# Kernel optimization log

Hardware: AMD Instinct MI355X
Metric: run time of the kernel (lower is better)

## Reference

```python
import jax, jax.numpy as jnp
import numpy as np

M = 28            # mask head resolution (mask_logit[i] is MxM)
NUM_CLASSES = 80  # max value of cls_idx (mask_image channel count)


def setup_inputs() -> dict:
    key = jax.random.key(0)
    k1, k2, k3, k4, k5, k6, k7 = jax.random.split(key, 7)
    N, H, W = 100, 800, 800
    cx = jax.random.uniform(k1, (N,), minval=0.0, maxval=float(W - 1))
    cy = jax.random.uniform(k2, (N,), minval=0.0, maxval=float(H - 1))
    bw = jax.random.uniform(k3, (N,), minval=20.0, maxval=300.0)
    bh = jax.random.uniform(k4, (N,), minval=20.0, maxval=300.0)
    mask_rois = jnp.stack([cx - bw / 2, cy - bh / 2, cx + bw / 2, cy + bh / 2], axis=1).astype(jnp.float32)
    cls_prob = jax.random.uniform(k5, (N,), dtype=jnp.float32)
    mask_prob = jax.random.normal(k6, (N, M, M), dtype=jnp.float32)
    cls_idx = jax.random.randint(k7, (N,), 1, NUM_CLASSES + 1, dtype=jnp.int32)
    return {"mask_rois": mask_rois, "cls_prob": cls_prob, "mask_prob": mask_prob,
            "cls_idx": cls_idx, "im_h": H, "im_w": W}


def _paste(logit, box, H, W):
    """Bilinear-paste an MxM logit into the full HxW image (== cv2.resize to (w,h)
    then placing at the box, evaluated directly on image pixel coords)."""
    x0, y0, x1, y1 = box[0], box[1], box[2], box[3]  # int32
    w = jnp.maximum(x1 - x0 + 1, 1).astype(jnp.float32)
    h = jnp.maximum(y1 - y0 + 1, 1).astype(jnp.float32)
    xs = jnp.arange(W, dtype=jnp.float32)
    ys = jnp.arange(H, dtype=jnp.float32)
    # cv2 bilinear mapping: src = (dst + 0.5) * (M / size) - 0.5, clamped at borders
    sx = jnp.clip((xs - x0.astype(jnp.float32) + 0.5) * (M / w) - 0.5, 0.0, M - 1.0)
    sy = jnp.clip((ys - y0.astype(jnp.float32) + 0.5) * (M / h) - 0.5, 0.0, M - 1.0)
    ix0 = jnp.floor(sx).astype(jnp.int32); ix1 = jnp.minimum(ix0 + 1, M - 1); fx = sx - ix0
    iy0 = jnp.floor(sy).astype(jnp.int32); iy1 = jnp.minimum(iy0 + 1, M - 1); fy = sy - iy0
    v00 = logit[iy0[:, None], ix0[None, :]]
    v01 = logit[iy0[:, None], ix1[None, :]]
    v10 = logit[iy1[:, None], ix0[None, :]]
    v11 = logit[iy1[:, None], ix1[None, :]]
    val = ((1 - fy)[:, None] * ((1 - fx)[None, :] * v00 + fx[None, :] * v01)
           + fy[:, None] * ((1 - fx)[None, :] * v10 + fx[None, :] * v11))
    xi = jnp.arange(W, dtype=jnp.int32)
    yi = jnp.arange(H, dtype=jnp.int32)
    inside_x = (xi >= jnp.maximum(x0, 0)) & (xi < jnp.minimum(x1 + 1, W))
    inside_y = (yi >= jnp.maximum(y0, 0)) & (yi < jnp.minimum(y1 + 1, H))
    inside = inside_y[:, None] & inside_x[None, :]
    return jnp.where(inside, val, 0.0), inside


def _forward(mask_rois, cls_prob, mask_prob, cls_idx, H, W, thr):
    N = mask_prob.shape[0]
    order = jnp.argsort(-cls_prob)                       # sort by score, descending
    boxes = mask_rois[order].astype(jnp.int32)
    logits = mask_prob[order]
    cls = cls_idx[order].astype(jnp.int32) - 1           # 0-based class ids
    pasted, inside = jax.vmap(lambda l, b: _paste(l, b, H, W))(logits, boxes)  # [N,H,W]

    def step(mask_image, xs):
        logit, ins, c = xs
        mask = (logit > 0) & ins                          # thresholded, in-image crop mask
        prev = mask_image[c]
        msum = jnp.sum(mask).astype(jnp.float32)
        ovl = jnp.sum(mask & prev).astype(jnp.float32)    # overlap with accumulated class mask
        keep = (msum > 0) & (ovl <= thr * msum)           # skip if ratio > threshold
        mask_image = mask_image.at[c].set(prev | (mask & keep))
        return mask_image, keep

    mask_image0 = jnp.zeros((NUM_CLASSES, H, W), dtype=bool)
    _, keep = jax.lax.scan(step, mask_image0, (pasted, inside, cls))

    # compact kept masks to the front (frame_id order); dropped boxes go to slot N (discarded)
    pos = jnp.where(keep, jnp.cumsum(keep.astype(jnp.int32)) - 1, N)
    energy = jnp.where(inside & keep[:, None, None], pasted, 0.0)
    full = jnp.zeros((N + 1, H, W), pasted.dtype).at[pos].set(energy)
    mask_energy = full[:N][None]                          # [1, N, H, W], kept masks first
    keep_inds = jnp.full((N + 1,), -1, jnp.int32).at[pos].set(
        jnp.where(keep, order.astype(jnp.int32), -1))[:N]
    return keep_inds, mask_energy


def reference(mask_rois, cls_prob, mask_prob, cls_idx, im_h, im_w):
    return _forward(mask_rois, cls_prob, mask_prob, cls_idx, int(im_h), int(im_w), 0.3)
```

## Files before the change

### kernel.cpp

```cpp
#include <hip/hip_runtime.h>

#define NINST 100
#define MLOG 28
#define IMG 800
#define LOGSZ (MLOG * MLOG)

#define OFF_ORDER 0
#define OFF_CLS   100
#define OFF_BOX   200
#define OFF_MSUM  600
#define OFF_SLOT  800
#define OFF_NK    900
#define OFF_NPAIR 901
#define OFF_MASK  1024
#define ROWW      12
#define MSTRIDE   (ROWW * 304)
#define OFF_PAIRS (OFF_MASK + NINST * MSTRIDE)
#define PAIR_CAP  512
#define ZTOT      (IMG * IMG * NINST / 4)
#define ZGRID     4096

__global__ __launch_bounds__(256) void k_raster(const float* __restrict__ mask_prob,
                                                const float* __restrict__ cls_prob,
                                                const float* __restrict__ rois,
                                                const int* __restrict__ cls_idx,
                                                int* __restrict__ ws) {
    int b = blockIdx.x, tid = threadIdx.x;
    __shared__ float s_p[NINST];
    __shared__ int s_order[NINST];
    __shared__ float lg[LOGSZ];
    __shared__ int red[256];
    if (tid < NINST) s_p[tid] = cls_prob[tid];
    __syncthreads();
    if (tid < NINST) {
        float p = s_p[tid];
        int r = 0;
        for (int j = 0; j < NINST; j++) {
            float q = s_p[j];
            r += (q > p) || (q == p && j < tid);
        }
        s_order[r] = tid;
    }
    __syncthreads();
    int n = b;
    int orig = s_order[n];
    int x0 = (int)rois[4 * orig], y0 = (int)rois[4 * orig + 1];
    int x1 = (int)rois[4 * orig + 2], y1 = (int)rois[4 * orig + 3];
    if (b == 0) {
        if (tid == 0) ws[OFF_NPAIR] = 0;
        if (tid < NINST) {
            int o = s_order[tid];
            ws[OFF_ORDER + tid] = o;
            ws[OFF_CLS + tid] = cls_idx[o] - 1;
#pragma unroll
            for (int k = 0; k < 4; k++)
                ws[OFF_BOX + 4 * tid + k] = (int)rois[4 * o + k];
        }
    }
    for (int i = tid; i < LOGSZ; i += 256) lg[i] = mask_prob[orig * LOGSZ + i];
    __syncthreads();
    int xs = max(x0, 0), xe = min(x1 + 1, IMG);
    int ys = max(y0, 0), ye = min(y1 + 1, IMG);
    int wx0 = xs >> 5, nw = ((xe + 31) >> 5) - wx0, nrows = ye - ys;
    float wf = fmaxf((float)(x1 - x0 + 1), 1.f), hf = fmaxf((float)(y1 - y0 + 1), 1.f);
    float rx = 28.f / wf, ry = 28.f / hf;
    unsigned* mb = (unsigned*)(ws + OFF_MASK) + n * MSTRIDE;
    int total = nrows * nw, cnt = 0;
    for (int t = tid; t < total; t += 256) {
        int row = t / nw, wc = t - row * nw;
        int y = ys + row;
        float sy = ((float)y - (float)y0 + 0.5f) * ry - 0.5f;
        sy = fminf(fmaxf(sy, 0.f), 27.f);
        int iy0 = (int)sy, iy1 = min(iy0 + 1, 27);
        float fy = sy - (float)iy0;
        const float* r0 = lg + iy0 * MLOG;
        const float* r1 = lg + iy1 * MLOG;
        unsigned bits = 0u;
        int xbase = (wx0 + wc) << 5;
        int j0 = max(xs - xbase, 0), j1 = min(xe - xbase, 32);
        for (int j = j0; j < j1; j++) {
            int xx = xbase + j;
            float sx = ((float)xx - (float)x0 + 0.5f) * rx - 0.5f;
            sx = fminf(fmaxf(sx, 0.f), 27.f);
            int ix0 = (int)sx, ix1 = min(ix0 + 1, 27);
            float fx = sx - (float)ix0;
            float val = (1.f - fy) * ((1.f - fx) * r0[ix0] + fx * r0[ix1]) +
                        fy * ((1.f - fx) * r1[ix0] + fx * r1[ix1]);
            bits |= (val > 0.f) ? (1u << j) : 0u;
        }
        mb[row * ROWW + wc] = bits;
        cnt += __popc(bits);
    }
    red[tid] = cnt;
    __syncthreads();
    for (int s = 128; s; s >>= 1) {
        if (tid < s) red[tid] += red[tid + s];
        __syncthreads();
    }
    if (tid == 0) ws[OFF_MSUM + n] = red[0];
}

__global__ __launch_bounds__(64) void k_pairs(int* __restrict__ ws) {
    int i = blockIdx.x, j = blockIdx.y, tid = threadIdx.x;
    if (i >= j) return;
    if (ws[OFF_CLS + i] != ws[OFF_CLS + j]) return;
    if (ws[OFF_MSUM + i] == 0 || ws[OFF_MSUM + j] == 0) return;
    const int* bi = ws + OFF_BOX + 4 * i;
    const int* bj = ws + OFF_BOX + 4 * j;
    int ixs = max(bi[0], 0), ixe = min(bi[2] + 1, IMG);
    int iys = max(bi[1], 0), iye = min(bi[3] + 1, IMG);
    int jxs = max(bj[0], 0), jxe = min(bj[2] + 1, IMG);
    int jys = max(bj[1], 0), jye = min(bj[3] + 1, IMG);
    if (!(ixs < jxe && jxs < ixe && iys < jye && jys < iye)) return;
    int iwx0 = ixs >> 5, jwx0 = jxs >> 5;
    int wlo = max(iwx0, jwx0);
    int whi = min((ixe + 31) >> 5, (jxe + 31) >> 5);
    int rlo = max(iys, jys), rhi = min(iye, jye);
    int nw = whi - wlo, nrows = rhi - rlo;
    const unsigned* mi = (const unsigned*)(ws + OFF_MASK) + i * MSTRIDE;
    const unsigned* mj = (const unsigned*)(ws + OFF_MASK) + j * MSTRIDE;
    int total = nrows * nw, cnt = 0;
    for (int t = tid; t < total; t += 64) {
        int row = t / nw, wc = t - row * nw;
        int y = rlo + row, w = wlo + wc;
        unsigned a = mi[(y - iys) * ROWW + (w - iwx0)];
        unsigned b = mj[(y - jys) * ROWW + (w - jwx0)];
        cnt += __popc(a & b);
    }
    for (int off = 32; off; off >>= 1) cnt += __shfl_down(cnt, off);
    if (tid == 0) {
        int k = atomicAdd(ws + OFF_NPAIR, 1);
        if (k < PAIR_CAP) {
            ws[OFF_PAIRS + 3 * k] = i;
            ws[OFF_PAIRS + 3 * k + 1] = j;
            ws[OFF_PAIRS + 3 * k + 2] = cnt;
        }
    }
}

__global__ __launch_bounds__(256) void k_scan_zero(int* __restrict__ ws, float* __restrict__ out) {
    int b = blockIdx.x, tid = threadIdx.x;
    if (b > 0) {
        float4* z = (float4*)(out + NINST);
        for (size_t pi = (size_t)(b - 1) * 256 + tid; pi < (size_t)ZTOT; pi += (size_t)ZGRID * 256)
            z[pi] = make_float4(0.f, 0.f, 0.f, 0.f);
        return;
    }
    __shared__ int s_box[4 * NINST];
    __shared__ int s_msum[NINST];
    __shared__ int s_keep[NINST];
    __shared__ int s_cand[32];
    __shared__ int s_ncand, s_sum, s_max, s_need;
    __shared__ int s_pi[PAIR_CAP], s_pj[PAIR_CAP], s_po[PAIR_CAP];
    __shared__ int red[256];
    for (int i = tid; i < NINST; i += 256) s_msum[i] = ws[OFF_MSUM + i];
    for (int i = tid; i < 4 * NINST; i += 256) s_box[i] = ws[OFF_BOX + i];
    int npair = min(ws[OFF_NPAIR], PAIR_CAP);
    for (int i = tid; i < npair; i += 256) {
        s_pi[i] = ws[OFF_PAIRS + 3 * i];
        s_pj[i] = ws[OFF_PAIRS + 3 * i + 1];
        s_po[i] = ws[OFF_PAIRS + 3 * i + 2];
    }
    const unsigned* maskbase = (const unsigned*)(ws + OFF_MASK);
    __syncthreads();

    for (int n = 0; n < NINST; n++) {
        if (tid == 0) { s_ncand = 0; s_sum = 0; s_max = 0; }
        __syncthreads();
        for (int q = tid; q < npair; q += 256) {
            if (s_pj[q] == n && s_keep[s_pi[q]]) {
                int k = atomicAdd(&s_ncand, 1);
                if (k < 32) s_cand[k] = s_pi[q];
                atomicAdd(&s_sum, s_po[q]);
                atomicMax(&s_max, s_po[q]);
            }
        }
        __syncthreads();
        if (tid == 0) {
            int msum = s_msum[n];
            float t = 0.3f * (float)msum;
            int keep, need = 0;
            if (s_ncand == 0 || (float)s_sum <= t) keep = (msum > 0);
            else if ((float)s_max > t) keep = 0;
            else { keep = 0; need = 1; }
            s_keep[n] = keep;
            s_need = need;
        }
        __syncthreads();
        if (s_need) {
            int nc = min(s_ncand, 32);
            int nxs = max(s_box[4 * n], 0), nxe = min(s_box[4 * n + 2] + 1, IMG);
            int nys = max(s_box[4 * n + 1], 0), nye = min(s_box[4 * n + 3] + 1, IMG);
            int wx0 = nxs >> 5, nw = ((nxe + 31) >> 5) - wx0, nrows = nye - nys;
            const unsigned* mn = maskbase + n * MSTRIDE;
            int total = nrows * nw, ovl = 0;
            for (int t2 = tid; t2 < total; t2 += 256) {
                int row = t2 / nw, wc = t2 - row * nw;
                unsigned bits = mn[row * ROWW + wc];
                if (!bits) continue;
                int y = nys + row, wa = wx0 + wc;
                unsigned img = 0;
                for (int k = 0; k < nc; k++) {
                    int m = s_cand[k];
                    int mys = max(s_box[4 * m + 1], 0), mye = min(s_box[4 * m + 3] + 1, IMG);
                    int mxs = max(s_box[4 * m], 0), mxe = min(s_box[4 * m + 2] + 1, IMG);
                    int mwx0 = mxs >> 5, mnw = ((mxe + 31) >> 5) - mwx0;
                    int rr = y - mys, cc = wa - mwx0;
                    if (rr >= 0 && rr < (mye - mys) && cc >= 0 && cc < mnw)
                        img |= maskbase[m * MSTRIDE + rr * ROWW + cc];
                }
                ovl += __popc(bits & img);
            }
            red[tid] = ovl;
            __syncthreads();
            for (int s = 128; s; s >>= 1) {
                if (tid < s) red[tid] += red[tid + s];
                __syncthreads();
            }
            if (tid == 0) {
                int msum = s_msum[n];
                s_keep[n] = (msum > 0) && ((float)red[0] <= 0.3f * (float)msum);
            }
        }
    }
    __syncthreads();
    if (tid == 0) {
        int nk = 0;
        for (int n = 0; n < NINST; n++) {
            if (s_keep[n]) {
                ws[OFF_SLOT + nk] = n;
                out[nk] = (float)ws[OFF_ORDER + n];
                nk++;
            }
        }
        ws[OFF_NK] = nk;
        for (int s = nk; s < NINST; s++) out[s] = -1.f;
    }
}

__global__ __launch_bounds__(256) void k_box(const float* __restrict__ mask_prob,
                                             const int* __restrict__ ws,
                                             float* __restrict__ out) {
    int slot = blockIdx.y, tid = threadIdx.x;
    if (slot >= ws[OFF_NK]) return;
    int n = ws[OFF_SLOT + slot];
    const int* box = ws + OFF_BOX + 4 * n;
    int x0 = box[0], y0 = box[1], x1 = box[2], y1 = box[3];
    int xs = max(x0, 0), xe = min(x1 + 1, IMG);
    int ys = max(y0, 0), ye = min(y1 + 1, IMG);
    int xa = xs & ~3;
    int w4 = (xe - xa + 3) >> 2;
    int rows = ye - ys;
    int total = rows * w4;
    __shared__ float lg[LOGSZ];
    int orig = ws[OFF_ORDER + n];
    for (int i = tid; i < LOGSZ; i += 256) lg[i] = mask_prob[orig * LOGSZ + i];
    __syncthreads();
    float wf = fmaxf((float)(x1 - x0 + 1), 1.f), hf = fmaxf((float)(y1 - y0 + 1), 1.f);
    float rx = 28.f / wf, ry = 28.f / hf;
    float* base = out + NINST + (size_t)slot * (IMG * IMG);
    for (int t = blockIdx.x * 256 + tid; t < total; t += gridDim.x * 256) {
        int row = t / w4, c4 = t - row * w4;
        int y = ys + row, xb = xa + (c4 << 2);
        float sy = ((float)y - (float)y0 + 0.5f) * ry - 0.5f;
        sy = fminf(fmaxf(sy, 0.f), 27.f);
        int iy0 = (int)sy, iy1 = min(iy0 + 1, 27);
        float fy = sy - (float)iy0;
        const float* r0 = lg + iy0 * MLOG;
        const float* r1 = lg + iy1 * MLOG;
        float v[4];
#pragma unroll
        for (int j = 0; j < 4; j++) {
            int xx = xb + j;
            float val = 0.f;
            if (xx >= xs && xx < xe) {
                float sx = ((float)xx - (float)x0 + 0.5f) * rx - 0.5f;
                sx = fminf(fmaxf(sx, 0.f), 27.f);
                int ix0 = (int)sx, ix1 = min(ix0 + 1, 27);
                float fx = sx - (float)ix0;
                val = (1.f - fy) * ((1.f - fx) * r0[ix0] + fx * r0[ix1]) +
                      fy * ((1.f - fx) * r1[ix0] + fx * r1[ix1]);
            }
            v[j] = val;
        }
        *(float4*)(base + (size_t)y * IMG + xb) = make_float4(v[0], v[1], v[2], v[3]);
    }
}

extern "C" void kernel_launch(void* const* d_in, const int* in_sizes, int n_in,
                              void* d_out, int out_size, void* d_ws, size_t ws_size,
                              hipStream_t stream) {
    const float* rois      = (const float*)d_in[0];
    const float* cls_prob  = (const float*)d_in[1];
    const float* mask_prob = (const float*)d_in[2];
    const int*   cls_idx   = (const int*)d_in[3];
    int* ws = (int*)d_ws;
    float* out = (float*)d_out;

    k_raster<<<dim3(NINST), dim3(256), 0, stream>>>(mask_prob, cls_prob, rois, cls_idx, ws);
    k_pairs<<<dim3(NINST, NINST), dim3(64), 0, stream>>>(ws);
    k_scan_zero<<<dim3(1 + ZGRID), dim3(256), 0, stream>>>(ws, out);
    k_box<<<dim3(91, NINST), dim3(256), 0, stream>>>(mask_prob, ws, out);
}
```

Before: 331.8 us.

## Fuse four kernels into one persistent kernel with grid-wide atomic barriers

Result: slower. 625.1 us (+88.4%).

```diff
diff --git a/kernel.cpp b/kernel.cpp
--- a/kernel.cpp
+++ b/kernel.cpp
@@ -12,278 +12,310 @@
 #define OFF_SLOT  800
 #define OFF_NK    900
 #define OFF_NPAIR 901
+#define OFF_BAR   904
 #define OFF_MASK  1024
 #define ROWW      12
 #define MSTRIDE   (ROWW * 304)
 #define OFF_PAIRS (OFF_MASK + NINST * MSTRIDE)
 #define PAIR_CAP  512
 #define ZTOT      (IMG * IMG * NINST / 4)
-#define ZGRID     4096
-
-__global__ __launch_bounds__(256) void k_raster(const float* __restrict__ mask_prob,
+#define GRID      1024
+#define BOXTILES  91
+#define BOXVTOT   (NINST * BOXTILES)
+#define BOXCHUNK  ((BOXVTOT + GRID - 1) / GRID)
+
+__device__ __forceinline__ void gbar(int* cnt) {
+    __syncthreads();
+    if (threadIdx.x == 0) {
+        __threadfence();
+        atomicAdd(cnt, 1);
+        while (__hip_atomic_load(cnt, __ATOMIC_RELAXED, __HIP_MEMORY_SCOPE_AGENT) < GRID)
+            __builtin_amdgcn_s_sleep(8);
+        __threadfence();
+    }
+    __syncthreads();
+}
+
+__global__ __launch_bounds__(256, 4) void k_all(const float* __restrict__ mask_prob,
                                                 const float* __restrict__ cls_prob,
                                                 const float* __restrict__ rois,
                                                 const int* __restrict__ cls_idx,
-                                                int* __restrict__ ws) {
+                                                int* __restrict__ ws,
+                                                float* __restrict__ out) {
     int b = blockIdx.x, tid = threadIdx.x;
     __shared__ float s_p[NINST];
     __shared__ int s_order[NINST];
     __shared__ float lg[LOGSZ];
     __shared__ int red[256];
-    if (tid < NINST) s_p[tid] = cls_prob[tid];
-    __syncthreads();
-    if (tid < NINST) {
-        float p = s_p[tid];
-        int r = 0;
-        for (int j = 0; j < NINST; j++) {
-            float q = s_p[j];
-            r += (q > p) || (q == p && j < tid);
-        }
-        s_order[r] = tid;
-    }
-    __syncthreads();
-    int n = b;
-    int orig = s_order[n];
-    int x0 = (int)rois[4 * orig], y0 = (int)rois[4 * orig + 1];
-    int x1 = (int)rois[4 * orig + 2], y1 = (int)rois[4 * orig + 3];
-    if (b == 0) {
-        if (tid == 0) ws[OFF_NPAIR] = 0;
-        if (tid < NINST) {
-            int o = s_order[tid];
-            ws[OFF_ORDER + tid] = o;
-            ws[OFF_CLS + tid] = cls_idx[o] - 1;
-#pragma unroll
-            for (int k = 0; k < 4; k++)
-                ws[OFF_BOX + 4 * tid + k] = (int)rois[4 * o + k];
-        }
-    }
-    for (int i = tid; i < LOGSZ; i += 256) lg[i] = mask_prob[orig * LOGSZ + i];
-    __syncthreads();
-    int xs = max(x0, 0), xe = min(x1 + 1, IMG);
-    int ys = max(y0, 0), ye = min(y1 + 1, IMG);
-    int wx0 = xs >> 5, nw = ((xe + 31) >> 5) - wx0, nrows = ye - ys;
-    float wf = fmaxf((float)(x1 - x0 + 1), 1.f), hf = fmaxf((float)(y1 - y0 + 1), 1.f);
-    float rx = 28.f / wf, ry = 28.f / hf;
-    unsigned* mb = (unsigned*)(ws + OFF_MASK) + n * MSTRIDE;
-    int total = nrows * nw, cnt = 0;
-    for (int t = tid; t < total; t += 256) {
-        int row = t / nw, wc = t - row * nw;
-        int y = ys + row;
-        float sy = ((float)y - (float)y0 + 0.5f) * ry - 0.5f;
-        sy = fminf(fmaxf(sy, 0.f), 27.f);
-        int iy0 = (int)sy, iy1 = min(iy0 + 1, 27);
-        float fy = sy - (float)iy0;
-        const float* r0 = lg + iy0 * MLOG;
-        const float* r1 = lg + iy1 * MLOG;
-        unsigned bits = 0u;
-        int xbase = (wx0 + wc) << 5;
-        int j0 = max(xs - xbase, 0), j1 = min(xe - xbase, 32);
-        for (int j = j0; j < j1; j++) {
-            int xx = xbase + j;
-            float sx = ((float)xx - (float)x0 + 0.5f) * rx - 0.5f;
-            sx = fminf(fmaxf(sx, 0.f), 27.f);
-            int ix0 = (int)sx, ix1 = min(ix0 + 1, 27);
-            float fx = sx - (float)ix0;
-            float val = (1.f - fy) * ((1.f - fx) * r0[ix0] + fx * r0[ix1]) +
-                        fy * ((1.f - fx) * r1[ix0] + fx * r1[ix1]);
-            bits |= (val > 0.f) ? (1u << j) : 0u;
-        }
-        mb[row * ROWW + wc] = bits;
-        cnt += __popc(bits);
-    }
-    red[tid] = cnt;
-    __syncthreads();
-    for (int s = 128; s; s >>= 1) {
-        if (tid < s) red[tid] += red[tid + s];
-        __syncthreads();
-    }
-    if (tid == 0) ws[OFF_MSUM + n] = red[0];
-}
-
-__global__ __launch_bounds__(64) void k_pairs(int* __restrict__ ws) {
-    int i = blockIdx.x, j = blockIdx.y, tid = threadIdx.x;
-    if (i >= j) return;
-    if (ws[OFF_CLS + i] != ws[OFF_CLS + j]) return;
-    if (ws[OFF_MSUM + i] == 0 || ws[OFF_MSUM + j] == 0) return;
-    const int* bi = ws + OFF_BOX + 4 * i;
-    const int* bj = ws + OFF_BOX + 4 * j;
-    int ixs = max(bi[0], 0), ixe = min(bi[2] + 1, IMG);
-    int iys = max(bi[1], 0), iye = min(bi[3] + 1, IMG);
-    int jxs = max(bj[0], 0), jxe = min(bj[2] + 1, IMG);
-    int jys = max(bj[1], 0), jye = min(bj[3] + 1, IMG);
-    if (!(ixs < jxe && jxs < ixe && iys < jye && jys < iye)) return;
-    int iwx0 = ixs >> 5, jwx0 = jxs >> 5;
-    int wlo = max(iwx0, jwx0);
-    int whi = min((ixe + 31) >> 5, (jxe + 31) >> 5);
-    int rlo = max(iys, jys), rhi = min(iye, jye);
-    int nw = whi - wlo, nrows = rhi - rlo;
-    const unsigned* mi = (const unsigned*)(ws + OFF_MASK) + i * MSTRIDE;
-    const unsigned* mj = (const unsigned*)(ws + OFF_MASK) + j * MSTRIDE;
-    int total = nrows * nw, cnt = 0;
-    for (int t = tid; t < total; t += 64) {
-        int row = t / nw, wc = t - row * nw;
-        int y = rlo + row, w = wlo + wc;
-        unsigned a = mi[(y - iys) * ROWW + (w - iwx0)];
-        unsigned b = mj[(y - jys) * ROWW + (w - jwx0)];
-        cnt += __popc(a & b);
-    }
-    for (int off = 32; off; off >>= 1) cnt += __shfl_down(cnt, off);
-    if (tid == 0) {
-        int k = atomicAdd(ws + OFF_NPAIR, 1);
-        if (k < PAIR_CAP) {
-            ws[OFF_PAIRS + 3 * k] = i;
-            ws[OFF_PAIRS + 3 * k + 1] = j;
-            ws[OFF_PAIRS + 3 * k + 2] = cnt;
-        }
-    }
-}
-
-__global__ __launch_bounds__(256) void k_scan_zero(int* __restrict__ ws, float* __restrict__ out) {
-    int b = blockIdx.x, tid = threadIdx.x;
-    if (b > 0) {
-        float4* z = (float4*)(out + NINST);
-        for (size_t pi = (size_t)(b - 1) * 256 + tid; pi < (size_t)ZTOT; pi += (size_t)ZGRID * 256)
-            z[pi] = make_float4(0.f, 0.f, 0.f, 0.f);
-        return;
-    }
     __shared__ int s_box[4 * NINST];
     __shared__ int s_msum[NINST];
     __shared__ int s_keep[NINST];
     __shared__ int s_cand[32];
     __shared__ int s_ncand, s_sum, s_max, s_need;
     __shared__ int s_pi[PAIR_CAP], s_pj[PAIR_CAP], s_po[PAIR_CAP];
-    __shared__ int red[256];
-    for (int i = tid; i < NINST; i += 256) s_msum[i] = ws[OFF_MSUM + i];
-    for (int i = tid; i < 4 * NINST; i += 256) s_box[i] = ws[OFF_BOX + i];
-    int npair = min(ws[OFF_NPAIR], PAIR_CAP);
-    for (int i = tid; i < npair; i += 256) {
-        s_pi[i] = ws[OFF_PAIRS + 3 * i];
-        s_pj[i] = ws[OFF_PAIRS + 3 * i + 1];
-        s_po[i] = ws[OFF_PAIRS + 3 * i + 2];
-    }
-    const unsigned* maskbase = (const unsigned*)(ws + OFF_MASK);
-    __syncthreads();
-
-    for (int n = 0; n < NINST; n++) {
-        if (tid == 0) { s_ncand = 0; s_sum = 0; s_max = 0; }
-        __syncthreads();
-        for (int q = tid; q < npair; q += 256) {
-            if (s_pj[q] == n && s_keep[s_pi[q]]) {
-                int k = atomicAdd(&s_ncand, 1);
-                if (k < 32) s_cand[k] = s_pi[q];
-                atomicAdd(&s_sum, s_po[q]);
-                atomicMax(&s_max, s_po[q]);
-            }
-        }
-        __syncthreads();
-        if (tid == 0) {
-            int msum = s_msum[n];
-            float t = 0.3f * (float)msum;
-            int keep, need = 0;
-            if (s_ncand == 0 || (float)s_sum <= t) keep = (msum > 0);
-            else if ((float)s_max > t) keep = 0;
-            else { keep = 0; need = 1; }
-            s_keep[n] = keep;
-            s_need = need;
-        }
-        __syncthreads();
-        if (s_need) {
-            int nc = min(s_ncand, 32);
-            int nxs = max(s_box[4 * n], 0), nxe = min(s_box[4 * n + 2] + 1, IMG);
-            int nys = max(s_box[4 * n + 1], 0), nye = min(s_box[4 * n + 3] + 1, IMG);
-            int wx0 = nxs >> 5, nw = ((nxe + 31) >> 5) - wx0, nrows = nye - nys;
-            const unsigned* mn = maskbase + n * MSTRIDE;
-            int total = nrows * nw, ovl = 0;
-            for (int t2 = tid; t2 < total; t2 += 256) {
-                int row = t2 / nw, wc = t2 - row * nw;
-                unsigned bits = mn[row * ROWW + wc];
-                if (!bits) continue;
-                int y = nys + row, wa = wx0 + wc;
-                unsigned img = 0;
-                for (int k = 0; k < nc; k++) {
-                    int m = s_cand[k];
-                    int mys = max(s_box[4 * m + 1], 0), mye = min(s_box[4 * m + 3] + 1, IMG);
-                    int mxs = max(s_box[4 * m], 0), mxe = min(s_box[4 * m + 2] + 1, IMG);
-                    int mwx0 = mxs >> 5, mnw = ((mxe + 31) >> 5) - mwx0;
-                    int rr = y - mys, cc = wa - mwx0;
-                    if (rr >= 0 && rr < (mye - mys) && cc >= 0 && cc < mnw)
-                        img |= maskbase[m * MSTRIDE + rr * ROWW + cc];
-                }
-                ovl += __popc(bits & img);
-            }
-            red[tid] = ovl;
-            __syncthreads();
-            for (int s = 128; s; s >>= 1) {
-                if (tid < s) red[tid] += red[tid + s];
-                __syncthreads();
-            }
-            if (tid == 0) {
-                int msum = s_msum[n];
-                s_keep[n] = (msum > 0) && ((float)red[0] <= 0.3f * (float)msum);
-            }
-        }
-    }
-    __syncthreads();
-    if (tid == 0) {
-        int nk = 0;
-        for (int n = 0; n < NINST; n++) {
-            if (s_keep[n]) {
-                ws[OFF_SLOT + nk] = n;
-                out[nk] = (float)ws[OFF_ORDER + n];
-                nk++;
-            }
-        }
-        ws[OFF_NK] = nk;
-        for (int s = nk; s < NINST; s++) out[s] = -1.f;
-    }
-}
-
-__global__ __launch_bounds__(256) void k_box(const float* __restrict__ mask_prob,
-                                             const int* __restrict__ ws,
-                                             float* __restrict__ out) {
-    int slot = blockIdx.y, tid = threadIdx.x;
-    if (slot >= ws[OFF_NK]) return;
-    int n = ws[OFF_SLOT + slot];
-    const int* box = ws + OFF_BOX + 4 * n;
-    int x0 = box[0], y0 = box[1], x1 = box[2], y1 = box[3];
-    int xs = max(x0, 0), xe = min(x1 + 1, IMG);
-    int ys = max(y0, 0), ye = min(y1 + 1, IMG);
-    int xa = xs & ~3;
-    int w4 = (xe - xa + 3) >> 2;
-    int rows = ye - ys;
-    int total = rows * w4;
-    __shared__ float lg[LOGSZ];
-    int orig = ws[OFF_ORDER + n];
-    for (int i = tid; i < LOGSZ; i += 256) lg[i] = mask_prob[orig * LOGSZ + i];
-    __syncthreads();
-    float wf = fmaxf((float)(x1 - x0 + 1), 1.f), hf = fmaxf((float)(y1 - y0 + 1), 1.f);
-    float rx = 28.f / wf, ry = 28.f / hf;
-    float* base = out + NINST + (size_t)slot * (IMG * IMG);
-    for (int t = blockIdx.x * 256 + tid; t < total; t += gridDim.x * 256) {
-        int row = t / w4, c4 = t - row * w4;
-        int y = ys + row, xb = xa + (c4 << 2);
-        float sy = ((float)y - (float)y0 + 0.5f) * ry - 0.5f;
-        sy = fminf(fmaxf(sy, 0.f), 27.f);
-        int iy0 = (int)sy, iy1 = min(iy0 + 1, 27);
-        float fy = sy - (float)iy0;
-        const float* r0 = lg + iy0 * MLOG;
-        const float* r1 = lg + iy1 * MLOG;
-        float v[4];
+
+    if (b < NINST) {
+        if (tid < NINST) s_p[tid] = cls_prob[tid];
+        __syncthreads();
+        if (tid < NINST) {
+            float p = s_p[tid];
+            int r = 0;
+            for (int j = 0; j < NINST; j++) {
+                float q = s_p[j];
+                r += (q > p) || (q == p && j < tid);
+            }
+            s_order[r] = tid;
+        }
+        __syncthreads();
+        int n = b;
+        int orig = s_order[n];
+        int x0 = (int)rois[4 * orig], y0 = (int)rois[4 * orig + 1];
+        int x1 = (int)rois[4 * orig + 2], y1 = (int)rois[4 * orig + 3];
+        if (b == 0) {
+            if (tid < NINST) {
+                int o = s_order[tid];
+                ws[OFF_ORDER + tid] = o;
+                ws[OFF_CLS + tid] = cls_idx[o] - 1;
 #pragma unroll
-        for (int j = 0; j < 4; j++) {
-            int xx = xb + j;
-            float val = 0.f;
-            if (xx >= xs && xx < xe) {
+                for (int k = 0; k < 4; k++)
+                    ws[OFF_BOX + 4 * tid + k] = (int)rois[4 * o + k];
+            }
+        }
+        for (int i = tid; i < LOGSZ; i += 256) lg[i] = mask_prob[orig * LOGSZ + i];
+        __syncthreads();
+        int xs = max(x0, 0), xe = min(x1 + 1, IMG);
+        int ys = max(y0, 0), ye = min(y1 + 1, IMG);
+        int wx0 = xs >> 5, nw = ((xe + 31) >> 5) - wx0, nrows = ye - ys;
+        float wf = fmaxf((float)(x1 - x0 + 1), 1.f), hf = fmaxf((float)(y1 - y0 + 1), 1.f);
+        float rx = 28.f / wf, ry = 28.f / hf;
+        unsigned* mb = (unsigned*)(ws + OFF_MASK) + n * MSTRIDE;
+        int total = nrows * nw, cnt = 0;
+        for (int t = tid; t < total; t += 256) {
+            int row = t / nw, wc = t - row * nw;
+            int y = ys + row;
+            float sy = ((float)y - (float)y0 + 0.5f) * ry - 0.5f;
+            sy = fminf(fmaxf(sy, 0.f), 27.f);
+            int iy0 = (int)sy, iy1 = min(iy0 + 1, 27);
+            float fy = sy - (float)iy0;
+            const float* r0 = lg + iy0 * MLOG;
+            const float* r1 = lg + iy1 * MLOG;
+            unsigned bits = 0u;
+            int xbase = (wx0 + wc) << 5;
+            int j0 = max(xs - xbase, 0), j1 = min(xe - xbase, 32);
+            for (int j = j0; j < j1; j++) {
+                int xx = xbase + j;
                 float sx = ((float)xx - (float)x0 + 0.5f) * rx - 0.5f;
                 sx = fminf(fmaxf(sx, 0.f), 27.f);
                 int ix0 = (int)sx, ix1 = min(ix0 + 1, 27);
                 float fx = sx - (float)ix0;
-                val = (1.f - fy) * ((1.f - fx) * r0[ix0] + fx * r0[ix1]) +
-                      fy * ((1.f - fx) * r1[ix0] + fx * r1[ix1]);
-            }
-            v[j] = val;
-        }
-        *(float4*)(base + (size_t)y * IMG + xb) = make_float4(v[0], v[1], v[2], v[3]);
+                float val = (1.f - fy) * ((1.f - fx) * r0[ix0] + fx * r0[ix1]) +
+                            fy * ((1.f - fx) * r1[ix0] + fx * r1[ix1]);
+                bits |= (val > 0.f) ? (1u << j) : 0u;
+            }
+            mb[row * ROWW + wc] = bits;
+            cnt += __popc(bits);
+        }
+        red[tid] = cnt;
+        __syncthreads();
+        for (int s = 128; s; s >>= 1) {
+            if (tid < s) red[tid] += red[tid + s];
+            __syncthreads();
+        }
+        if (tid == 0) ws[OFF_MSUM + n] = red[0];
+    }
+    gbar(ws + OFF_BAR + 0);
+
+    {
+        int wid = (b << 2) | (tid >> 6), lane = tid & 63;
+        for (int idx = wid; idx < NINST * NINST; idx += (GRID << 2)) {
+            int i = idx / NINST, j = idx - i * NINST;
+            if (i >= j) continue;
+            if (ws[OFF_CLS + i] != ws[OFF_CLS + j]) continue;
+            if (ws[OFF_MSUM + i] == 0 || ws[OFF_MSUM + j] == 0) continue;
+            const int* bi = ws + OFF_BOX + 4 * i;
+            const int* bj = ws + OFF_BOX + 4 * j;
+            int ixs = max(bi[0], 0), ixe = min(bi[2] + 1, IMG);
+            int iys = max(bi[1], 0), iye = min(bi[3] + 1, IMG);
+            int jxs = max(bj[0], 0), jxe = min(bj[2] + 1, IMG);
+            int jys = max(bj[1], 0), jye = min(bj[3] + 1, IMG);
+            if (!(ixs < jxe && jxs < ixe && iys < jye && jys < iye)) continue;
+            int iwx0 = ixs >> 5, jwx0 = jxs >> 5;
+            int wlo = max(iwx0, jwx0);
+            int whi = min((ixe + 31) >> 5, (jxe + 31) >> 5);
+            int rlo = max(iys, jys), rhi = min(iye, jye);
+            int nw = whi - wlo, nrows = rhi - rlo;
+            const unsigned* mi = (const unsigned*)(ws + OFF_MASK) + i * MSTRIDE;
+            const unsigned* mj = (const unsigned*)(ws + OFF_MASK) + j * MSTRIDE;
+            int total = nrows * nw, cnt = 0;
+            for (int t = lane; t < total; t += 64) {
+                int row = t / nw, wc = t - row * nw;
+                int y = rlo + row, w = wlo + wc;
+                unsigned a = mi[(y - iys) * ROWW + (w - iwx0)];
+                unsigned bb = mj[(y - jys) * ROWW + (w - jwx0)];
+                cnt += __popc(a & bb);
+            }
+            for (int off = 32; off; off >>= 1) cnt += __shfl_down(cnt, off);
+            if (lane == 0) {
+                int k = atomicAdd(ws + OFF_NPAIR, 1);
+                if (k < PAIR_CAP) {
+                    ws[OFF_PAIRS + 3 * k] = i;
+                    ws[OFF_PAIRS + 3 * k + 1] = j;
+                    ws[OFF_PAIRS + 3 * k + 2] = cnt;
+                }
+            }
+        }
+    }
+    gbar(ws + OFF_BAR + 1);
+
+    if (b > 0) {
+        float4* z = (float4*)(out + NINST);
+        for (size_t pi = (size_t)(b - 1) * 256 + tid; pi < (size_t)ZTOT; pi += (size_t)(GRID - 1) * 256)
+            z[pi] = make_float4(0.f, 0.f, 0.f, 0.f);
+    } else {
+        for (int i = tid; i < NINST; i += 256) s_msum[i] = ws[OFF_MSUM + i];
+        for (int i = tid; i < 4 * NINST; i += 256) s_box[i] = ws[OFF_BOX + i];
+        int npair = min(ws[OFF_NPAIR], PAIR_CAP);
+        for (int i = tid; i < npair; i += 256) {
+            s_pi[i] = ws[OFF_PAIRS + 3 * i];
+            s_pj[i] = ws[OFF_PAIRS + 3 * i + 1];
+            s_po[i] = ws[OFF_PAIRS + 3 * i + 2];
+        }
+        const unsigned* maskbase = (const unsigned*)(ws + OFF_MASK);
+        __syncthreads();
+        for (int n = 0; n < NINST; n++) {
+            if (tid == 0) { s_ncand = 0; s_sum = 0; s_max = 0; }
+            __syncthreads();
+            for (int q = tid; q < npair; q += 256) {
+                if (s_pj[q] == n && s_keep[s_pi[q]]) {
+                    int k = atomicAdd(&s_ncand, 1);
+                    if (k < 32) s_cand[k] = s_pi[q];
+                    atomicAdd(&s_sum, s_po[q]);
+                    atomicMax(&s_max, s_po[q]);
+                }
+            }
+            __syncthreads();
+            if (tid == 0) {
+                int msum = s_msum[n];
+                float t = 0.3f * (float)msum;
+                int keep, need = 0;
+                if (s_ncand == 0 || (float)s_sum <= t) keep = (msum > 0);
+                else if ((float)s_max > t) keep = 0;
+                else { keep = 0; need = 1; }
+                s_keep[n] = keep;
+                s_need = need;
+            }
+            __syncthreads();
+            if (s_need) {
+                int nc = min(s_ncand, 32);
+                int nxs = max(s_box[4 * n], 0), nxe = min(s_box[4 * n + 2] + 1, IMG);
+                int nys = max(s_box[4 * n + 1], 0), nye = min(s_box[4 * n + 3] + 1, IMG);
+                int wx0 = nxs >> 5, nw = ((nxe + 31) >> 5) - wx0, nrows = nye - nys;
+                const unsigned* mn = maskbase + n * MSTRIDE;
+                int total = nrows * nw, ovl = 0;
+                for (int t2 = tid; t2 < total; t2 += 256) {
+                    int row = t2 / nw, wc = t2 - row * nw;
+                    unsigned bits = mn[row * ROWW + wc];
+                    if (!bits) continue;
+                    int y = nys + row, wa = wx0 + wc;
+                    unsigned img = 0;
+                    for (int k = 0; k < nc; k++) {
+                        int m = s_cand[k];
+                        int mys = max(s_box[4 * m + 1], 0), mye = min(s_box[4 * m + 3] + 1, IMG);
+                        int mxs = max(s_box[4 * m], 0), mxe = min(s_box[4 * m + 2] + 1, IMG);
+                        int mwx0 = mxs >> 5, mnw = ((mxe + 31) >> 5) - mwx0;
+                        int rr = y - mys, cc = wa - mwx0;
+                        if (rr >= 0 && rr < (mye - mys) && cc >= 0 && cc < mnw)
+                            img |= maskbase[m * MSTRIDE + rr * ROWW + cc];
+                    }
+                    ovl += __popc(bits & img);
+                }
+                red[tid] = ovl;
+                __syncthreads();
+                for (int s = 128; s; s >>= 1) {
+                    if (tid < s) red[tid] += red[tid + s];
+                    __syncthreads();
+                }
+                if (tid == 0) {
+                    int msum = s_msum[n];
+                    s_keep[n] = (msum > 0) && ((float)red[0] <= 0.3f * (float)msum);
+                }
+            }
+        }
+        __syncthreads();
+        if (tid == 0) {
+            int nk = 0;
+            for (int n = 0; n < NINST; n++) {
+                if (s_keep[n]) {
+                    ws[OFF_SLOT + nk] = n;
+                    out[nk] = (float)ws[OFF_ORDER + n];
+                    nk++;
+                }
+            }
+            ws[OFF_NK] = nk;
+            for (int s = nk; s < NINST; s++) out[s] = -1.f;
+        }
+    }
+    gbar(ws + OFF_BAR + 2);
+
+    {
+        int nk = ws[OFF_NK];
+        int v0 = b * BOXCHUNK;
+        int v1 = min(v0 + BOXCHUNK, BOXVTOT);
+        int cur = -1;
+        int x0 = 0, y0 = 0, x1 = 0, xs = 0, xe = 0, ys = 0, xa = 0, w4 = 0, total = 0;
+        float rx = 0.f, ry = 0.f;
+        float* base = out;
+        for (int v = v0; v < v1; v++) {
+            int slot = v / BOXTILES, tile = v - slot * BOXTILES;
+            if (slot >= nk) continue;
+            if (slot != cur) {
+                cur = slot;
+                int n = ws[OFF_SLOT + slot];
+                const int* box = ws + OFF_BOX + 4 * n;
+                x0 = box[0]; y0 = box[1]; x1 = box[2];
+                int yy1 = box[3];
+                xs = max(x0, 0); xe = min(x1 + 1, IMG);
+                ys = max(y0, 0);
+                int ye = min(yy1 + 1, IMG);
+                xa = xs & ~3;
+                w4 = (xe - xa + 3) >> 2;
+                total = (ye - ys) * w4;
+                int orig = ws[OFF_ORDER + n];
+                __syncthreads();
+                for (int i = tid; i < LOGSZ; i += 256) lg[i] = mask_prob[orig * LOGSZ + i];
+                __syncthreads();
+                rx = 28.f / fmaxf((float)(x1 - x0 + 1), 1.f);
+                ry = 28.f / fmaxf((float)(yy1 - y0 + 1), 1.f);
+                base = out + NINST + (size_t)slot * (IMG * IMG);
+            }
+            int p = tile * 256 + tid;
+            if (p < total) {
+                int row = p / w4, c4 = p - row * w4;
+                int y = ys + row, xb = xa + (c4 << 2);
+                float sy = ((float)y - (float)y0 + 0.5f) * ry - 0.5f;
+                sy = fminf(fmaxf(sy, 0.f), 27.f);
+                int iy0 = (int)sy, iy1 = min(iy0 + 1, 27);
+                float fy = sy - (float)iy0;
+                const float* r0 = lg + iy0 * MLOG;
+                const float* r1 = lg + iy1 * MLOG;
+                float vq[4];
+#pragma unroll
+                for (int j = 0; j < 4; j++) {
+                    int xx = xb + j;
+                    float val = 0.f;
+                    if (xx >= xs && xx < xe) {
+                        float sx = ((float)xx - (float)x0 + 0.5f) * rx - 0.5f;
+                        sx = fminf(fmaxf(sx, 0.f), 27.f);
+                        int ix0 = (int)sx, ix1 = min(ix0 + 1, 27);
+                        float fx = sx - (float)ix0;
+                        val = (1.f - fy) * ((1.f - fx) * r0[ix0] + fx * r0[ix1]) +
+                              fy * ((1.f - fx) * r1[ix0] + fx * r1[ix1]);
+                    }
+                    vq[j] = val;
+                }
+                *(float4*)(base + (size_t)y * IMG + xb) = make_float4(vq[0], vq[1], vq[2], vq[3]);
+            }
+        }
     }
 }
 
@@ -297,8 +329,6 @@
     int* ws = (int*)d_ws;
     float* out = (float*)d_out;
 
-    k_raster<<<dim3(NINST), dim3(256), 0, stream>>>(mask_prob, cls_prob, rois, cls_idx, ws);
-    k_pairs<<<dim3(NINST, NINST), dim3(64), 0, stream>>>(ws);
-    k_scan_zero<<<dim3(1 + ZGRID), dim3(256), 0, stream>>>(ws, out);
-    k_box<<<dim3(91, NINST), dim3(256), 0, stream>>>(mask_prob, ws, out);
+    hipMemsetAsync(ws + OFF_NK, 0, 8 * sizeof(int), stream);
+    k_all<<<dim3(GRID), dim3(256), 0, stream>>>(mask_prob, cls_prob, rois, cls_idx, ws, out);
 }
```

## Fuse zero-fill and box paste into one kernel gated by a device flag

Applied to the files above, without the earlier changes.

Measured after the change: 357.8 us. 7.8% more time.

```diff
diff --git a/kernel.cpp b/kernel.cpp
--- a/kernel.cpp
+++ b/kernel.cpp
@@ -12,13 +12,16 @@
 #define OFF_SLOT  800
 #define OFF_NK    900
 #define OFF_NPAIR 901
+#define OFF_FLAG  904
 #define OFF_MASK  1024
 #define ROWW      12
 #define MSTRIDE   (ROWW * 304)
 #define OFF_PAIRS (OFF_MASK + NINST * MSTRIDE)
 #define PAIR_CAP  512
-#define ZTOT      (IMG * IMG * NINST / 4)
-#define ZGRID     4096
+#define SLOTSZ    (IMG * IMG)
+#define SUBB      40
+#define ROWSPB    (IMG / SUBB)
+#define MEGAGRID  (1 + NINST * SUBB)
 
 __global__ __launch_bounds__(256) void k_raster(const float* __restrict__ mask_prob,
                                                 const float* __restrict__ cls_prob,
@@ -47,7 +50,6 @@
     int x0 = (int)rois[4 * orig], y0 = (int)rois[4 * orig + 1];
     int x1 = (int)rois[4 * orig + 2], y1 = (int)rois[4 * orig + 3];
     if (b == 0) {
-        if (tid == 0) ws[OFF_NPAIR] = 0;
         if (tid < NINST) {
             int o = s_order[tid];
             ws[OFF_ORDER + tid] = o;
@@ -100,50 +102,112 @@
     if (tid == 0) ws[OFF_MSUM + n] = red[0];
 }
 
-__global__ __launch_bounds__(64) void k_pairs(int* __restrict__ ws) {
-    int i = blockIdx.x, j = blockIdx.y, tid = threadIdx.x;
-    if (i >= j) return;
-    if (ws[OFF_CLS + i] != ws[OFF_CLS + j]) return;
-    if (ws[OFF_MSUM + i] == 0 || ws[OFF_MSUM + j] == 0) return;
-    const int* bi = ws + OFF_BOX + 4 * i;
-    const int* bj = ws + OFF_BOX + 4 * j;
-    int ixs = max(bi[0], 0), ixe = min(bi[2] + 1, IMG);
-    int iys = max(bi[1], 0), iye = min(bi[3] + 1, IMG);
-    int jxs = max(bj[0], 0), jxe = min(bj[2] + 1, IMG);
-    int jys = max(bj[1], 0), jye = min(bj[3] + 1, IMG);
-    if (!(ixs < jxe && jxs < ixe && iys < jye && jys < iye)) return;
-    int iwx0 = ixs >> 5, jwx0 = jxs >> 5;
-    int wlo = max(iwx0, jwx0);
-    int whi = min((ixe + 31) >> 5, (jxe + 31) >> 5);
-    int rlo = max(iys, jys), rhi = min(iye, jye);
-    int nw = whi - wlo, nrows = rhi - rlo;
-    const unsigned* mi = (const unsigned*)(ws + OFF_MASK) + i * MSTRIDE;
-    const unsigned* mj = (const unsigned*)(ws + OFF_MASK) + j * MSTRIDE;
-    int total = nrows * nw, cnt = 0;
-    for (int t = tid; t < total; t += 64) {
-        int row = t / nw, wc = t - row * nw;
-        int y = rlo + row, w = wlo + wc;
-        unsigned a = mi[(y - iys) * ROWW + (w - iwx0)];
-        unsigned b = mj[(y - jys) * ROWW + (w - jwx0)];
-        cnt += __popc(a & b);
-    }
-    for (int off = 32; off; off >>= 1) cnt += __shfl_down(cnt, off);
-    if (tid == 0) {
-        int k = atomicAdd(ws + OFF_NPAIR, 1);
-        if (k < PAIR_CAP) {
-            ws[OFF_PAIRS + 3 * k] = i;
-            ws[OFF_PAIRS + 3 * k + 1] = j;
-            ws[OFF_PAIRS + 3 * k + 2] = cnt;
+__global__ __launch_bounds__(256) void k_pairs(int* __restrict__ ws) {
+    int b = blockIdx.x, tid = threadIdx.x;
+    int wid = (b << 2) | (tid >> 6), lane = tid & 63;
+    for (int idx = wid; idx < NINST * NINST; idx += (128 << 2)) {
+        int i = idx / NINST, j = idx - i * NINST;
+        if (i >= j) continue;
+        if (ws[OFF_CLS + i] != ws[OFF_CLS + j]) continue;
+        if (ws[OFF_MSUM + i] == 0 || ws[OFF_MSUM + j] == 0) continue;
+        const int* bi = ws + OFF_BOX + 4 * i;
+        const int* bj = ws + OFF_BOX + 4 * j;
+        int ixs = max(bi[0], 0), ixe = min(bi[2] + 1, IMG);
+        int iys = max(bi[1], 0), iye = min(bi[3] + 1, IMG);
+        int jxs = max(bj[0], 0), jxe = min(bj[2] + 1, IMG);
+        int jys = max(bj[1], 0), jye = min(bj[3] + 1, IMG);
+        if (!(ixs < jxe && jxs < ixe && iys < jye && jys < iye)) continue;
+        int iwx0 = ixs >> 5, jwx0 = jxs >> 5;
+        int wlo = max(iwx0, jwx0);
+        int whi = min((ixe + 31) >> 5, (jxe + 31) >> 5);
+        int rlo = max(iys, jys), rhi = min(iye, jye);
+        int nw = whi - wlo, nrows = rhi - rlo;
+        const unsigned* mi = (const unsigned*)(ws + OFF_MASK) + i * MSTRIDE;
+        const unsigned* mj = (const unsigned*)(ws + OFF_MASK) + j * MSTRIDE;
+        int total = nrows * nw, cnt = 0;
+        for (int t = lane; t < total; t += 64) {
+            int row = t / nw, wc = t - row * nw;
+            int y = rlo + row, w = wlo + wc;
+            unsigned a = mi[(y - iys) * ROWW + (w - iwx0)];
+            unsigned bb = mj[(y - jys) * ROWW + (w - jwx0)];
+            cnt += __popc(a & bb);
+        }
+        for (int off = 32; off; off >>= 1) cnt += __shfl_down(cnt, off);
+        if (lane == 0) {
+            int k = atomicAdd(ws + OFF_NPAIR, 1);
+            if (k < PAIR_CAP) {
+                ws[OFF_PAIRS + 3 * k] = i;
+                ws[OFF_PAIRS + 3 * k + 1] = j;
+                ws[OFF_PAIRS + 3 * k + 2] = cnt;
+            }
         }
     }
 }
 
-__global__ __launch_bounds__(256) void k_scan_zero(int* __restrict__ ws, float* __restrict__ out) {
+__global__ __launch_bounds__(256) void k_mega(const float* __restrict__ mask_prob,
+                                              int* __restrict__ ws,
+                                              float* __restrict__ out) {
     int b = blockIdx.x, tid = threadIdx.x;
     if (b > 0) {
-        float4* z = (float4*)(out + NINST);
-        for (size_t pi = (size_t)(b - 1) * 256 + tid; pi < (size_t)ZTOT; pi += (size_t)ZGRID * 256)
-            z[pi] = make_float4(0.f, 0.f, 0.f, 0.f);
+        int s = (b - 1) / SUBB, sub = (b - 1) - s * SUBB;
+        int r0 = sub * ROWSPB;
+        float* base = out + NINST + (size_t)s * SLOTSZ + (size_t)r0 * IMG;
+        float4* z = (float4*)base;
+        for (int t = tid; t < (ROWSPB * IMG / 4); t += 256)
+            z[t] = make_float4(0.f, 0.f, 0.f, 0.f);
+        __syncthreads();
+        if (tid == 0) {
+            while (__hip_atomic_load(ws + OFF_FLAG, __ATOMIC_RELAXED,
+                                     __HIP_MEMORY_SCOPE_AGENT) == 0)
+                __builtin_amdgcn_s_sleep(32);
+            __builtin_amdgcn_fence(__ATOMIC_ACQUIRE, "agent");
+        }
+        __syncthreads();
+        int nk = ws[OFF_NK];
+        if (s >= nk) return;
+        int n = ws[OFF_SLOT + s];
+        const int* box = ws + OFF_BOX + 4 * n;
+        int x0 = box[0], y0 = box[1], x1 = box[2], y1 = box[3];
+        int xs = max(x0, 0), xe = min(x1 + 1, IMG);
+        int ys = max(y0, 0), ye = min(y1 + 1, IMG);
+        int ya = max(ys, r0), yb = min(ye, r0 + ROWSPB);
+        if (ya >= yb) return;
+        __shared__ float lg[LOGSZ];
+        int orig = ws[OFF_ORDER + n];
+        for (int i = tid; i < LOGSZ; i += 256) lg[i] = mask_prob[orig * LOGSZ + i];
+        __syncthreads();
+        int xa = xs & ~3;
+        int w4 = (xe - xa + 3) >> 2;
+        int nrows = yb - ya, total = nrows * w4;
+        float rx = 28.f / fmaxf((float)(x1 - x0 + 1), 1.f);
+        float ry = 28.f / fmaxf((float)(y1 - y0 + 1), 1.f);
+        float* sbase = out + NINST + (size_t)s * SLOTSZ;
+        for (int t = tid; t < total; t += 256) {
+            int row = t / w4, c4 = t - row * w4;
+            int y = ya + row, xb = xa + (c4 << 2);
+            float sy = ((float)y - (float)y0 + 0.5f) * ry - 0.5f;
+            sy = fminf(fmaxf(sy, 0.f), 27.f);
+            int iy0 = (int)sy, iy1 = min(iy0 + 1, 27);
+            float fy = sy - (float)iy0;
+            const float* rr0 = lg + iy0 * MLOG;
+            const float* rr1 = lg + iy1 * MLOG;
+            float vq[4];
+#pragma unroll
+            for (int j = 0; j < 4; j++) {
+                int xx = xb + j;
+                float val = 0.f;
+                if (xx >= xs && xx < xe) {
+                    float sx = ((float)xx - (float)x0 + 0.5f) * rx - 0.5f;
+                    sx = fminf(fmaxf(sx, 0.f), 27.f);
+                    int ix0 = (int)sx, ix1 = min(ix0 + 1, 27);
+                    float fx = sx - (float)ix0;
+                    val = (1.f - fy) * ((1.f - fx) * rr0[ix0] + fx * rr0[ix1]) +
+                          fy * ((1.f - fx) * rr1[ix0] + fx * rr1[ix1]);
+                }
+                vq[j] = val;
+            }
+            *(float4*)(sbase + (size_t)y * IMG + xb) = make_float4(vq[0], vq[1], vq[2], vq[3]);
+        }
         return;
     }
     __shared__ int s_box[4 * NINST];
@@ -163,7 +227,6 @@
     }
     const unsigned* maskbase = (const unsigned*)(ws + OFF_MASK);
     __syncthreads();
-
     for (int n = 0; n < NINST; n++) {
         if (tid == 0) { s_ncand = 0; s_sum = 0; s_max = 0; }
         __syncthreads();
@@ -235,55 +298,9 @@
         }
         ws[OFF_NK] = nk;
         for (int s = nk; s < NINST; s++) out[s] = -1.f;
-    }
-}
-
-__global__ __launch_bounds__(256) void k_box(const float* __restrict__ mask_prob,
-                                             const int* __restrict__ ws,
-                                             float* __restrict__ out) {
-    int slot = blockIdx.y, tid = threadIdx.x;
-    if (slot >= ws[OFF_NK]) return;
-    int n = ws[OFF_SLOT + slot];
-    const int* box = ws + OFF_BOX + 4 * n;
-    int x0 = box[0], y0 = box[1], x1 = box[2], y1 = box[3];
-    int xs = max(x0, 0), xe = min(x1 + 1, IMG);
-    int ys = max(y0, 0), ye = min(y1 + 1, IMG);
-    int xa = xs & ~3;
-    int w4 = (xe - xa + 3) >> 2;
-    int rows = ye - ys;
-    int total = rows * w4;
-    __shared__ float lg[LOGSZ];
-    int orig = ws[OFF_ORDER + n];
-    for (int i = tid; i < LOGSZ; i += 256) lg[i] = mask_prob[orig * LOGSZ + i];
-    __syncthreads();
-    float wf = fmaxf((float)(x1 - x0 + 1), 1.f), hf = fmaxf((float)(y1 - y0 + 1), 1.f);
-    float rx = 28.f / wf, ry = 28.f / hf;
-    float* base = out + NINST + (size_t)slot * (IMG * IMG);
-    for (int t = blockIdx.x * 256 + tid; t < total; t += gridDim.x * 256) {
-        int row = t / w4, c4 = t - row * w4;
-        int y = ys + row, xb = xa + (c4 << 2);
-        float sy = ((float)y - (float)y0 + 0.5f) * ry - 0.5f;
-        sy = fminf(fmaxf(sy, 0.f), 27.f);
-        int iy0 = (int)sy, iy1 = min(iy0 + 1, 27);
-        float fy = sy - (float)iy0;
-        const float* r0 = lg + iy0 * MLOG;
-        const float* r1 = lg + iy1 * MLOG;
-        float v[4];
-#pragma unroll
-        for (int j = 0; j < 4; j++) {
-            int xx = xb + j;
-            float val = 0.f;
-            if (xx >= xs && xx < xe) {
-                float sx = ((float)xx - (float)x0 + 0.5f) * rx - 0.5f;
-                sx = fminf(fmaxf(sx, 0.f), 27.f);
-                int ix0 = (int)sx, ix1 = min(ix0 + 1, 27);
-                float fx = sx - (float)ix0;
-                val = (1.f - fy) * ((1.f - fx) * r0[ix0] + fx * r0[ix1]) +
-                      fy * ((1.f - fx) * r1[ix0] + fx * r1[ix1]);
-            }
-            v[j] = val;
-        }
-        *(float4*)(base + (size_t)y * IMG + xb) = make_float4(v[0], v[1], v[2], v[3]);
+        __builtin_amdgcn_fence(__ATOMIC_RELEASE, "agent");
+        __hip_atomic_store(ws + OFF_FLAG, 1, __ATOMIC_RELAXED,
+                           __HIP_MEMORY_SCOPE_AGENT);
     }
 }
 
@@ -297,8 +314,8 @@
     int* ws = (int*)d_ws;
     float* out = (float*)d_out;
 
+    hipMemsetAsync(ws + OFF_NK, 0, 8 * sizeof(int), stream);
     k_raster<<<dim3(NINST), dim3(256), 0, stream>>>(mask_prob, cls_prob, rois, cls_idx, ws);
-    k_pairs<<<dim3(NINST, NINST), dim3(64), 0, stream>>>(ws);
-    k_scan_zero<<<dim3(1 + ZGRID), dim3(256), 0, stream>>>(ws, out);
-    k_box<<<dim3(91, NINST), dim3(256), 0, stream>>>(mask_prob, ws, out);
+    k_pairs<<<dim3(128), dim3(256), 0, stream>>>(ws);
+    k_mega<<<dim3(MEGAGRID), dim3(256), 0, stream>>>(mask_prob, ws, out);
 }
```
